# Performance work log

Hardware: AMD Instinct MI355X
Metric: run time of the kernel (lower is better)

Reference implementation:

```python
import jax, jax.numpy as jnp
import numpy as np

NUM_HEADS = 16
TOP_K = 64


def setup_inputs() -> dict:
    key = jax.random.key(0)
    ks = jax.random.split(key, 9)
    B, S, E = 2, 1024, 1024
    x = jax.random.normal(ks[0], (B, S, E), jnp.float32)
    init = lambda k: jax.random.normal(k, (E, E), jnp.float32) * 0.02
    return {
        "x": x,
        "Wq": init(ks[1]), "bq": jnp.zeros((E,), jnp.float32),
        "Wk": init(ks[2]), "bk": jnp.zeros((E,), jnp.float32),
        "Wv": init(ks[3]), "bv": jnp.zeros((E,), jnp.float32),
        "Wo": init(ks[4]), "bo": jnp.zeros((E,), jnp.float32),
    }


def reference(x, Wq, bq, Wk, bk, Wv, bv, Wo, bo):
    B, S, E = x.shape
    H = NUM_HEADS
    hd = E // H
    scale = jnp.sqrt(jnp.float32(hd))

    def proj(W, b):  # torch nn.Linear: y = x @ W^T + b -> [B,H,S,hd]
        return (x @ W.T + b).reshape(B, S, H, hd).transpose(0, 2, 1, 3)

    q = proj(Wq, bq)
    k = proj(Wk, bk)
    v = proj(Wv, bv)

    # full scores, then per-query top-k selection (same math as the torch per-i loop)
    scores = jnp.einsum('bhqd,bhkd->bhqk', q, k) / scale          # [B,H,S,S]
    top_scores, top_idx = jax.lax.top_k(scores, TOP_K)            # [B,H,S,K]

    # gather top-k values: vg[b,h,q,j,:] = v[b,h, top_idx[b,h,q,j], :]
    vg = jnp.take_along_axis(v[:, :, None, :, :], top_idx[..., None], axis=3)  # [B,H,S,K,hd]

    # torch recomputes q . gathered_k / scale, which equals top_scores exactly
    w = jax.nn.softmax(top_scores, axis=-1)                       # [B,H,S,K]
    out = jnp.einsum('bhqk,bhqkd->bhqd', w, vg)                   # [B,H,S,hd]

    out = out.transpose(0, 2, 1, 3).reshape(B, S, E)
    return out @ Wo.T + bo
```

## Files before the change

kernel.cpp:

```cpp
#include <hip/hip_runtime.h>
#include <hip/hip_bf16.h>
#include <stdint.h>


typedef __bf16 bf16_t;
typedef bf16_t bf16x8 __attribute__((ext_vector_type(8)));
typedef bf16_t bf16x4 __attribute__((ext_vector_type(4)));
typedef float  f32x4  __attribute__((ext_vector_type(4)));

#define NB 2
#define SS 1024
#define EE 1024
#define NH 16
#define HD 64
#define NBH (NB*NH)
#define NX_ ((size_t)NB*SS*EE)
#define NW_ ((size_t)EE*EE)

__device__ __forceinline__ f32x4 mfma16(bf16x8 a, bf16x8 b, f32x4 c) {
  return __builtin_amdgcn_mfma_f32_16x16x32_bf16(a, b, c, 0, 0, 0);
}

__device__ __forceinline__ void split3(float x, bf16_t& h, bf16_t& m, bf16_t& l) {
  h = (bf16_t)x;
  float r = x - (float)h;
  m = (bf16_t)r;
  float r2 = r - (float)m;
  l = (bf16_t)r2;
}

__device__ __forceinline__ void wave_fence() {
  __builtin_amdgcn_wave_barrier();
  __builtin_amdgcn_s_waitcnt(0);
  __builtin_amdgcn_wave_barrier();
}

__device__ __forceinline__ void gld16(const bf16_t* g, bf16_t* l) {
  __builtin_amdgcn_global_load_lds(
      (const __attribute__((address_space(1))) void*)g,
      (__attribute__((address_space(3))) void*)l, 16, 0, 0);
}

__global__ __launch_bounds__(256) void presplit_all(
    const float* __restrict__ x,  const float* __restrict__ wq,
    const float* __restrict__ wk, const float* __restrict__ wv,
    const float* __restrict__ wo, bf16_t* __restrict__ base)
{
  const int blk = blockIdx.x;
  const float* src; bf16_t* h; size_t n; int i;
  if (blk < 2048)      { src = x;  h = base;                   n = NX_; i = blk;        }
  else if (blk < 3072) { src = wq; h = base + 3*NX_;           n = NW_; i = blk - 2048; }
  else if (blk < 4096) { src = wk; h = base + 3*NX_ + 3*NW_;   n = NW_; i = blk - 3072; }
  else if (blk < 5120) { src = wv; h = base + 3*NX_ + 6*NW_;   n = NW_; i = blk - 4096; }
  else                 { src = wo; h = base + 3*NX_ + 9*NW_;   n = NW_; i = blk - 5120; }
  bf16_t* m = h + n;
  bf16_t* l = m + n;
  int idx = i * 256 + threadIdx.x;
  float4 v = ((const float4*)src)[idx];
  float t[4] = { v.x, v.y, v.z, v.w };
  bf16x4 hv, mv, lv;
#pragma unroll
  for (int j = 0; j < 4; j++) {
    bf16_t a, b, c;
    split3(t[j], a, b, c);
    hv[j] = a; mv[j] = b; lv[j] = c;
  }
  ((bf16x4*)h)[idx] = hv;
  ((bf16x4*)m)[idx] = mv;
  ((bf16x4*)l)[idx] = lv;
}

__global__ __launch_bounds__(256, 2) void gemm_qk(
    const bf16_t* __restrict__ Ah, const bf16_t* __restrict__ Am,
    const bf16_t* __restrict__ Al,
    const bf16_t* __restrict__ Bqh, const bf16_t* __restrict__ Bqm,
    const bf16_t* __restrict__ Bql,
    const bf16_t* __restrict__ Bkh, const bf16_t* __restrict__ Bkm,
    const bf16_t* __restrict__ Bkl,
    const float* __restrict__ biasq, const float* __restrict__ biask,
    bf16_t* __restrict__ qH, bf16_t* __restrict__ qM, bf16_t* __restrict__ qL,
    bf16_t* __restrict__ kH, bf16_t* __restrict__ kM, bf16_t* __restrict__ kL)
{
  __shared__ bf16_t As[3][128 * 32];
  __shared__ bf16_t Bs[3][64 * 32];

  const int z = blockIdx.z;
  const bf16_t* AP[3] = { Ah, Am, Al };
  const bf16_t* BP[3] = { z ? Bkh : Bqh, z ? Bkm : Bqm, z ? Bkl : Bql };
  const float* bias = z ? biask : biasq;
  bf16_t* dH = z ? kH : qH;
  bf16_t* dM = z ? kM : qM;
  bf16_t* dL = z ? kL : qL;

  const int tid  = threadIdx.x;
  const int wv   = tid >> 6, lane = tid & 63;
  const int quad = lane >> 4, l16 = lane & 15;
  const int m0 = blockIdx.y * 128, n0 = blockIdx.x * 64;
  const int wm = (wv & 1) * 64, wn = (wv >> 1) * 32;

  const int arow = wv * 32 + (lane >> 2);
  const int brow = wv * 16 + (lane >> 2);
  const int q8   = (lane & 3) * 8;
  const size_t aoff0 = (size_t)(m0 + arow) * 1024 + q8;
  const size_t boff  = (size_t)(n0 + brow) * 1024 + q8;

  f32x4 accH0[4][2] = {};
  f32x4 accH1[4][2] = {};
  f32x4 accC [4][2] = {};

  for (int k0 = 0; k0 < 1024; k0 += 32) {
    __syncthreads();
#pragma unroll
    for (int L = 0; L < 3; L++) {
      gld16(AP[L] + aoff0 + k0,              &As[L][(wv * 32) * 32]);
      gld16(AP[L] + aoff0 + 16 * 1024 + k0,  &As[L][(wv * 32 + 16) * 32]);
      gld16(BP[L] + boff + k0,               &Bs[L][(wv * 16) * 32]);
    }
    __syncthreads();

    bf16x8 bfr[2][3];
#pragma unroll
    for (int nt = 0; nt < 2; nt++)
#pragma unroll
      for (int L = 0; L < 3; L++)
        bfr[nt][L] = *(const bf16x8*)&Bs[L][(wn + nt * 16 + l16) * 32 + quad * 8];

    const bool hi = (k0 >= 512);
#pragma unroll
    for (int mt = 0; mt < 4; mt++) {
      bf16x8 af[3];
#pragma unroll
      for (int L = 0; L < 3; L++)
        af[L] = *(const bf16x8*)&As[L][(wm + mt * 16 + l16) * 32 + quad * 8];
#pragma unroll
      for (int nt = 0; nt < 2; nt++) {
        f32x4& H = hi ? accH1[mt][nt] : accH0[mt][nt];
        H = mfma16(af[0], bfr[nt][0], H);
        f32x4 c = accC[mt][nt];
        c = mfma16(af[0], bfr[nt][1], c);
        c = mfma16(af[1], bfr[nt][0], c);
        c = mfma16(af[0], bfr[nt][2], c);
        c = mfma16(af[2], bfr[nt][0], c);
        c = mfma16(af[1], bfr[nt][1], c);
        accC[mt][nt] = c;
      }
    }
  }

#pragma unroll
  for (int mt = 0; mt < 4; mt++)
#pragma unroll
  for (int nt = 0; nt < 2; nt++)
#pragma unroll
  for (int r  = 0; r  < 4;  r++) {
    int gm = m0 + wm + mt * 16 + quad * 4 + r;
    int gn = n0 + wn + nt * 16 + l16;
    float v = (accH0[mt][nt][r] + accH1[mt][nt][r]) + accC[mt][nt][r] + bias[gn];
    int b_ = gm >> 10, s_ = gm & 1023, h_ = gn >> 6, d_ = gn & 63;
    size_t di = (((size_t)b_ * NH + h_) * SS + s_) * HD + d_;
    bf16_t hh, mm, ll;
    split3(v, hh, mm, ll);
    dH[di] = hh; dM[di] = mm; dL[di] = ll;
  }
}

template<int MODE>
__global__ __launch_bounds__(256, 4) void gemm_nl2(
    const bf16_t* __restrict__ Ah, const bf16_t* __restrict__ Am,
    const bf16_t* __restrict__ Bh, const bf16_t* __restrict__ Bm,
    const float* __restrict__ bias, float* __restrict__ dF)
{
  __shared__ bf16_t As[2][64 * 32];
  __shared__ bf16_t Bs[2][64 * 32];

  const bf16_t* AP[2] = { Ah, Am };
  const bf16_t* BP[2] = { Bh, Bm };

  const int tid  = threadIdx.x;
  const int wv   = tid >> 6, lane = tid & 63;
  const int quad = lane >> 4, l16 = lane & 15;
  const int m0 = blockIdx.y * 64, n0 = blockIdx.x * 64;
  const int wm = (wv & 1) * 32, wn = (wv >> 1) * 32;

  const int srow = wv * 16 + (lane >> 2);
  const int q8   = (lane & 3) * 8;
  const size_t aoff = (size_t)(m0 + srow) * 1024 + q8;
  const size_t boff = (size_t)(n0 + srow) * 1024 + q8;

  f32x4 accH0[2][2] = {};
  f32x4 accH1[2][2] = {};
  f32x4 accC [2][2] = {};

  for (int k0 = 0; k0 < 1024; k0 += 32) {
    __syncthreads();
#pragma unroll
    for (int L = 0; L < 2; L++) {
      gld16(AP[L] + aoff + k0, &As[L][(wv * 16) * 32]);
      gld16(BP[L] + boff + k0, &Bs[L][(wv * 16) * 32]);
    }
    __syncthreads();

    bf16x8 bfr[2][2];
#pragma unroll
    for (int nt = 0; nt < 2; nt++)
#pragma unroll
      for (int L = 0; L < 2; L++)
        bfr[nt][L] = *(const bf16x8*)&Bs[L][(wn + nt * 16 + l16) * 32 + quad * 8];

    const bool hi = (k0 >= 512);
#pragma unroll
    for (int mt = 0; mt < 2; mt++) {
      bf16x8 af[2];
#pragma unroll
      for (int L = 0; L < 2; L++)
        af[L] = *(const bf16x8*)&As[L][(wm + mt * 16 + l16) * 32 + quad * 8];
#pragma unroll
      for (int nt = 0; nt < 2; nt++) {
        f32x4& H = hi ? accH1[mt][nt] : accH0[mt][nt];
        H = mfma16(af[0], bfr[nt][0], H);
        f32x4 c = accC[mt][nt];
        c = mfma16(af[0], bfr[nt][1], c);
        c = mfma16(af[1], bfr[nt][0], c);
        accC[mt][nt] = c;
      }
    }
  }

#pragma unroll
  for (int mt = 0; mt < 2; mt++)
#pragma unroll
  for (int nt = 0; nt < 2; nt++)
#pragma unroll
  for (int r  = 0; r  < 4;  r++) {
    int gm = m0 + wm + mt * 16 + quad * 4 + r;
    int gn = n0 + wn + nt * 16 + l16;
    float v = (accH0[mt][nt][r] + accH1[mt][nt][r]) + accC[mt][nt][r] + bias[gn];
    if (MODE == 2) {
      dF[(size_t)gm * 1024 + gn] = v;
    } else {
      int b_ = gm >> 10, s_ = gm & 1023, h_ = gn >> 6, d_ = gn & 63;
      dF[(((size_t)b_ * NH + h_) * SS + s_) * HD + d_] = v;
    }
  }
}

__global__ __launch_bounds__(512, 8) void attn_topk(
    const bf16_t* __restrict__ qhg, const bf16_t* __restrict__ qmg,
    const bf16_t* __restrict__ qlg,
    const bf16_t* __restrict__ khg, const bf16_t* __restrict__ kmg,
    const bf16_t* __restrict__ klg,
    const float*  __restrict__ vg,
    bf16_t* __restrict__ attnH, bf16_t* __restrict__ attnM)
{
  __shared__ float  sc[16 * 516];
  __shared__ float  selW[16 * 64];
  __shared__ ushort selI[16 * 64];

  const int tid  = threadIdx.x;
  const int wv   = tid >> 6, lane = tid & 63;
  const int quad = lane >> 4, l16 = lane & 15;
  const int xcd = blockIdx.x & 7;
  const int g   = blockIdx.x >> 3;
  const int bh  = xcd + 8 * (g >> 6);
  const int qt  = g & 63;
  const int b_ = bh >> 4, h_ = bh & 15;
  const int q0 = qt * 16;

  const size_t qbase = ((size_t)bh * SS + q0 + l16) * HD + quad * 8;
  bf16x8 aH[2], aM[2], aL[2];
#pragma unroll
  for (int ks = 0; ks < 2; ks++) {
    aH[ks] = *(const bf16x8*)(qhg + qbase + ks * 32);
    aM[ks] = *(const bf16x8*)(qmg + qbase + ks * 32);
    aL[ks] = *(const bf16x8*)(qlg + qbase + ks * 32);
  }

  float fv[2][16];
#pragma unroll
  for (int c = 0; c < 2; c++) {
    const size_t kwb = ((size_t)bh * SS + c * 512 + wv * 64 + l16) * HD + quad * 8;
#pragma unroll
    for (int t2 = 0; t2 < 4; t2++) {
      const size_t kb = kwb + (size_t)t2 * 16 * HD;
      bf16x8 bH0 = *(const bf16x8*)(khg + kb);
      bf16x8 bH1 = *(const bf16x8*)(khg + kb + 32);
      bf16x8 bM0 = *(const bf16x8*)(kmg + kb);
      bf16x8 bM1 = *(const bf16x8*)(kmg + kb + 32);
      bf16x8 bL0 = *(const bf16x8*)(klg + kb);
      bf16x8 bL1 = *(const bf16x8*)(klg + kb + 32);
      f32x4 accA = {}, accB = {}, accC = {};
      accA = mfma16(aH[0], bH0, accA);
      accB = mfma16(aH[1], bH1, accB);
      accC = mfma16(aH[0], bM0, accC);
      accC = mfma16(aH[1], bM1, accC);
      accC = mfma16(aM[0], bH0, accC);
      accC = mfma16(aM[1], bH1, accC);
      accC = mfma16(aH[0], bL0, accC);
      accC = mfma16(aH[1], bL1, accC);
      accC = mfma16(aL[0], bH0, accC);
      accC = mfma16(aL[1], bH1, accC);
      accC = mfma16(aM[0], bM0, accC);
      accC = mfma16(aM[1], bM1, accC);
      int key = wv * 64 + t2 * 16 + l16;
#pragma unroll
      for (int r = 0; r < 4; r++)
        sc[(quad * 4 + r) * 516 + key] = ((accA[r] + accB[r]) + accC[r]) * 0.125f;
    }
    __syncthreads();
#pragma unroll
    for (int i = 0; i < 8; i++) {
      fv[0][c * 8 + i] = sc[wv * 516 + i * 64 + lane];
      fv[1][c * 8 + i] = sc[(wv + 8) * 516 + i * 64 + lane];
    }
    __syncthreads();
  }

  uint32_t* bins  = (uint32_t*)sc + wv * 516;
  float*    candV = (float*)bins;
  ushort*   candI = (ushort*)(bins + 64);

  const uint64_t lt = (1ull << lane) - 1ull;
  for (int qi = 0; qi < 2; qi++) {
    int q = qi * 8 + wv;
    const float* fq = fv[qi];
    *(uint4*)(bins + lane * 8)     = uint4{0, 0, 0, 0};
    *(uint4*)(bins + lane * 8 + 4) = uint4{0, 0, 0, 0};
    wave_fence();
#pragma unroll
    for (int i = 0; i < 16; i++) {
      int b = (int)fmaxf(0.f, fminf(511.f, fmaf(fq[i], 32.f, 256.f)));
      atomicAdd(bins + b, 1u);
    }
    wave_fence();
    int base = 504 - 8 * lane;
    uint4 h0 = *(const uint4*)(bins + base);
    uint4 h1 = *(const uint4*)(bins + base + 4);
    uint32_t s_l = h0.x + h0.y + h0.z + h0.w + h1.x + h1.y + h1.z + h1.w;
    uint32_t x = s_l;
#pragma unroll
    for (int off = 1; off < 64; off <<= 1) {
      uint32_t y = __shfl_up(x, off);
      if (lane >= off) x += y;
    }
    uint32_t P = x - s_l;
    uint32_t harr[8] = { h1.w, h1.z, h1.y, h1.x, h0.w, h0.z, h0.y, h0.x };
    uint32_t cb = P, G = 0;
    int foundc = -1;
#pragma unroll
    for (int c = 0; c < 8; c++) {
      uint32_t hc = harr[c];
      if (foundc < 0 && (int)cb < 64 && (int)(cb + hc) >= 64) { foundc = c; G = cb; }
      cb += hc;
    }
    uint64_t fm = __ballot(foundc >= 0);
    int src   = __ffsll((unsigned long long)fm) - 1;
    int Bstar = __shfl((foundc >= 0) ? (511 - 8 * lane - foundc) : 0, src);
    int Gs    = __shfl((int)G, src);
    int needed = 64 - Gs;
    wave_fence();

    int pos = 0, cT = 0;
#pragma unroll
    for (int i = 0; i < 16; i++) {
      int b = (int)fmaxf(0.f, fminf(511.f, fmaf(fq[i], 32.f, 256.f)));
      bool hi = b > Bstar;
      bool cd = (b == Bstar);
      uint64_t hm = __ballot(hi);
      uint64_t em = __ballot(cd);
      int p  = pos + (int)__popcll(hm & lt);
      int cp = cT  + (int)__popcll(em & lt);
      if (hi) { selW[q * 64 + p] = fq[i]; selI[q * 64 + p] = (ushort)(i * 64 + lane); }
      if (cd && cp < 64) { candV[cp] = fq[i]; candI[cp] = (ushort)(i * 64 + lane); }
      pos += (int)__popcll(hm);
      cT  += (int)__popcll(em);
    }
    wave_fence();
    int C = cT < 64 ? cT : 64;
    float mv = candV[lane];
    int   mi = candI[lane];
    int rank = 0;
    for (int i = 0; i < C; i++) {
      float ov = candV[i]; int oi = candI[i];
      rank += (ov > mv || (ov == mv && oi < mi)) ? 1 : 0;
    }
    bool take = (lane < C) && (rank < needed);
    uint64_t tm = __ballot(take);
    int slot = Gs + (int)__popcll(tm & lt);
    if (take) { selW[q * 64 + slot] = mv; selI[q * 64 + slot] = (ushort)mi; }
    wave_fence();
    float sv = selW[q * 64 + lane];
    float mx = sv;
#pragma unroll
    for (int off = 32; off >= 1; off >>= 1) mx = fmaxf(mx, __shfl_xor(mx, off));
    float e = __expf(sv - mx);
    float sum = e;
#pragma unroll
    for (int off = 32; off >= 1; off >>= 1) sum += __shfl_xor(sum, off);
    selW[q * 64 + lane] = e / sum;
    wave_fence();
  }
  __syncthreads();

  {
    int q = tid >> 5, jh = (tid >> 4) & 1, dblk = (tid & 15) * 4;
    const float* vb = vg + (size_t)bh * SS * HD;
    f32x4 a4 = {};
#pragma unroll
    for (int bch = 0; bch < 2; bch++) {
      float wreg[16]; int ireg[16];
#pragma unroll
      for (int j = 0; j < 16; j++) {
        int jj = jh * 32 + bch * 16 + j;
        wreg[j] = selW[q * 64 + jj];
        ireg[j] = selI[q * 64 + jj];
      }
#pragma unroll
      for (int j = 0; j < 16; j++) {
        f32x4 v4 = *(const f32x4*)(vb + (size_t)ireg[j] * HD + dblk);
        a4 += wreg[j] * v4;
      }
    }
#pragma unroll
    for (int c = 0; c < 4; c++) a4[c] += __shfl_xor(a4[c], 16);
    if (jh == 0) {
      size_t dofs = ((size_t)b_ * SS + q0 + q) * EE + h_ * HD + dblk;
      bf16x4 oh, om;
#pragma unroll
      for (int j = 0; j < 4; j++) {
        bf16_t hh = (bf16_t)a4[j];
        oh[j] = hh;
        om[j] = (bf16_t)(a4[j] - (float)hh);
      }
      *(bf16x4*)(attnH + dofs) = oh;
      *(bf16x4*)(attnM + dofs) = om;
    }
  }
}

extern "C" void kernel_launch(void* const* d_in, const int* in_sizes, int n_in,
                              void* d_out, int out_size, void* d_ws, size_t ws_size,
                              hipStream_t stream)
{
  const float* x  = (const float*)d_in[0];
  const float* Wq = (const float*)d_in[1];
  const float* bq = (const float*)d_in[2];
  const float* Wk = (const float*)d_in[3];
  const float* bk = (const float*)d_in[4];
  const float* Wv = (const float*)d_in[5];
  const float* bv = (const float*)d_in[6];
  const float* Wo = (const float*)d_in[7];
  const float* bo = (const float*)d_in[8];

  bf16_t* base = (bf16_t*)d_ws;
  bf16_t *xh = base,            *xm = xh + NX_,  *xl = xm + NX_;
  bf16_t *wqh = base + 3*NX_,           *wqm = wqh + NW_, *wql = wqm + NW_;
  bf16_t *wkh = base + 3*NX_ + 3*NW_,   *wkm = wkh + NW_, *wkl = wkm + NW_;
  bf16_t *wvh = base + 3*NX_ + 6*NW_,   *wvm = wvh + NW_;
  bf16_t *woh = base + 3*NX_ + 9*NW_,   *wom = woh + NW_;
  bf16_t *p2 = base + 3*NX_ + 12*NW_;
  bf16_t *qh = p2,          *qm = qh + NX_, *ql = qm + NX_;
  bf16_t *kh = ql + NX_,    *km = kh + NX_, *kl = km + NX_;
  float  *vws = (float*)(kl + NX_);
  bf16_t *ath = (bf16_t*)(vws + NX_), *atm = ath + NX_;

  dim3 blk(256);
  presplit_all<<<dim3(6144), blk, 0, stream>>>(x, Wq, Wk, Wv, Wo, base);

  gemm_qk<<<dim3(EE / 64, (NB * SS) / 128, 2), blk, 0, stream>>>(
      xh, xm, xl, wqh, wqm, wql, wkh, wkm, wkl, bq, bk,
      qh, qm, ql, kh, km, kl);

  gemm_nl2<1><<<dim3(EE / 64, (NB * SS) / 64), blk, 0, stream>>>(
      xh, xm, wvh, wvm, bv, vws);

  attn_topk<<<dim3(NBH * (SS / 16)), dim3(512), 0, stream>>>(
      qh, qm, ql, kh, km, kl, vws, ath, atm);

  gemm_nl2<2><<<dim3(EE / 64, (NB * SS) / 64), blk, 0, stream>>>(
      ath, atm, woh, wom, bo, (float*)d_out);
}
```

Measured before the change: 381.7 us.

## Use 1024-thread blocks in attn_topk with one query per wave

The top-k attention kernel now launches 16 waves per block instead of 8. Each wave computes half as many score tiles and handles a single query in the selection phase, where before it looped over two. The value-gather phase splits the 64 selected keys four ways across lanes and reduces with two shuffles. K/Q offsets use 32-bit arithmetic. This adds intra-block parallelism and lowers per-thread register use, in exchange for larger blocks, more barrier participants and possibly lower block-level occupancy.

```diff
diff --git a/kernel.cpp b/kernel.cpp
--- a/kernel.cpp
+++ b/kernel.cpp
@@ -244,7 +244,7 @@
   }
 }
 
-__global__ __launch_bounds__(512, 8) void attn_topk(
+__global__ __launch_bounds__(1024, 4) void attn_topk(
     const bf16_t* __restrict__ qhg, const bf16_t* __restrict__ qmg,
     const bf16_t* __restrict__ qlg,
     const bf16_t* __restrict__ khg, const bf16_t* __restrict__ kmg,
@@ -266,7 +266,7 @@
   const int b_ = bh >> 4, h_ = bh & 15;
   const int q0 = qt * 16;
 
-  const size_t qbase = ((size_t)bh * SS + q0 + l16) * HD + quad * 8;
+  const uint32_t qbase = ((uint32_t)bh * SS + q0 + l16) * HD + quad * 8;
   bf16x8 aH[2], aM[2], aL[2];
 #pragma unroll
   for (int ks = 0; ks < 2; ks++) {
@@ -275,43 +275,45 @@
     aL[ks] = *(const bf16x8*)(qlg + qbase + ks * 32);
   }
 
-  float fv[2][16];
+  float fv[16];
 #pragma unroll
   for (int c = 0; c < 2; c++) {
-    const size_t kwb = ((size_t)bh * SS + c * 512 + wv * 64 + l16) * HD + quad * 8;
-#pragma unroll
-    for (int t2 = 0; t2 < 4; t2++) {
-      const size_t kb = kwb + (size_t)t2 * 16 * HD;
-      bf16x8 bH0 = *(const bf16x8*)(khg + kb);
-      bf16x8 bH1 = *(const bf16x8*)(khg + kb + 32);
-      bf16x8 bM0 = *(const bf16x8*)(kmg + kb);
-      bf16x8 bM1 = *(const bf16x8*)(kmg + kb + 32);
-      bf16x8 bL0 = *(const bf16x8*)(klg + kb);
-      bf16x8 bL1 = *(const bf16x8*)(klg + kb + 32);
-      f32x4 accA = {}, accB = {}, accC = {};
-      accA = mfma16(aH[0], bH0, accA);
-      accB = mfma16(aH[1], bH1, accB);
-      accC = mfma16(aH[0], bM0, accC);
-      accC = mfma16(aH[1], bM1, accC);
-      accC = mfma16(aM[0], bH0, accC);
-      accC = mfma16(aM[1], bH1, accC);
-      accC = mfma16(aH[0], bL0, accC);
-      accC = mfma16(aH[1], bL1, accC);
-      accC = mfma16(aL[0], bH0, accC);
-      accC = mfma16(aL[1], bH1, accC);
-      accC = mfma16(aM[0], bM0, accC);
-      accC = mfma16(aM[1], bM1, accC);
-      int key = wv * 64 + t2 * 16 + l16;
+    const uint32_t kwb = ((uint32_t)bh * SS + c * 512 + wv * 32 + l16) * HD + quad * 8;
+#pragma unroll
+    for (int t2 = 0; t2 < 2; t2++) {
+      const uint32_t kb = kwb + (uint32_t)t2 * 16 * HD;
+      f32x4 accH = {}, accC = {};
+      {
+        bf16x8 bH = *(const bf16x8*)(khg + kb);
+        bf16x8 bM = *(const bf16x8*)(kmg + kb);
+        bf16x8 bL = *(const bf16x8*)(klg + kb);
+        accH = mfma16(aH[0], bH, accH);
+        accC = mfma16(aH[0], bM, accC);
+        accC = mfma16(aM[0], bH, accC);
+        accC = mfma16(aH[0], bL, accC);
+        accC = mfma16(aL[0], bH, accC);
+        accC = mfma16(aM[0], bM, accC);
+      }
+      {
+        bf16x8 bH = *(const bf16x8*)(khg + kb + 32);
+        bf16x8 bM = *(const bf16x8*)(kmg + kb + 32);
+        bf16x8 bL = *(const bf16x8*)(klg + kb + 32);
+        accH = mfma16(aH[1], bH, accH);
+        accC = mfma16(aH[1], bM, accC);
+        accC = mfma16(aM[1], bH, accC);
+        accC = mfma16(aH[1], bL, accC);
+        accC = mfma16(aL[1], bH, accC);
+        accC = mfma16(aM[1], bM, accC);
+      }
+      int key = wv * 32 + t2 * 16 + l16;
 #pragma unroll
       for (int r = 0; r < 4; r++)
-        sc[(quad * 4 + r) * 516 + key] = ((accA[r] + accB[r]) + accC[r]) * 0.125f;
-    }
-    __syncthreads();
-#pragma unroll
-    for (int i = 0; i < 8; i++) {
-      fv[0][c * 8 + i] = sc[wv * 516 + i * 64 + lane];
-      fv[1][c * 8 + i] = sc[(wv + 8) * 516 + i * 64 + lane];
-    }
+        sc[(quad * 4 + r) * 516 + key] = (accH[r] + accC[r]) * 0.125f;
+    }
+    __syncthreads();
+#pragma unroll
+    for (int i = 0; i < 8; i++)
+      fv[c * 8 + i] = sc[wv * 516 + i * 64 + lane];
     __syncthreads();
   }
 
@@ -320,15 +322,14 @@
   ushort*   candI = (ushort*)(bins + 64);
 
   const uint64_t lt = (1ull << lane) - 1ull;
-  for (int qi = 0; qi < 2; qi++) {
-    int q = qi * 8 + wv;
-    const float* fq = fv[qi];
+  const int q = wv;
+  {
     *(uint4*)(bins + lane * 8)     = uint4{0, 0, 0, 0};
     *(uint4*)(bins + lane * 8 + 4) = uint4{0, 0, 0, 0};
     wave_fence();
 #pragma unroll
     for (int i = 0; i < 16; i++) {
-      int b = (int)fmaxf(0.f, fminf(511.f, fmaf(fq[i], 32.f, 256.f)));
+      int b = (int)fmaxf(0.f, fminf(511.f, fmaf(fv[i], 32.f, 256.f)));
       atomicAdd(bins + b, 1u);
     }
     wave_fence();
@@ -362,15 +363,15 @@
     int pos = 0, cT = 0;
 #pragma unroll
     for (int i = 0; i < 16; i++) {
-      int b = (int)fmaxf(0.f, fminf(511.f, fmaf(fq[i], 32.f, 256.f)));
+      int b = (int)fmaxf(0.f, fminf(511.f, fmaf(fv[i], 32.f, 256.f)));
       bool hi = b > Bstar;
       bool cd = (b == Bstar);
       uint64_t hm = __ballot(hi);
       uint64_t em = __ballot(cd);
       int p  = pos + (int)__popcll(hm & lt);
       int cp = cT  + (int)__popcll(em & lt);
-      if (hi) { selW[q * 64 + p] = fq[i]; selI[q * 64 + p] = (ushort)(i * 64 + lane); }
-      if (cd && cp < 64) { candV[cp] = fq[i]; candI[cp] = (ushort)(i * 64 + lane); }
+      if (hi) { selW[q * 64 + p] = fv[i]; selI[q * 64 + p] = (ushort)(i * 64 + lane); }
+      if (cd && cp < 64) { candV[cp] = fv[i]; candI[cp] = (ushort)(i * 64 + lane); }
       pos += (int)__popcll(hm);
       cT  += (int)__popcll(em);
     }
@@ -397,33 +398,32 @@
 #pragma unroll
     for (int off = 32; off >= 1; off >>= 1) sum += __shfl_xor(sum, off);
     selW[q * 64 + lane] = e / sum;
-    wave_fence();
   }
   __syncthreads();
 
   {
-    int q = tid >> 5, jh = (tid >> 4) & 1, dblk = (tid & 15) * 4;
+    int q2 = tid >> 6, jq = (tid >> 4) & 3, dblk = (tid & 15) * 4;
     const float* vb = vg + (size_t)bh * SS * HD;
     f32x4 a4 = {};
-#pragma unroll
-    for (int bch = 0; bch < 2; bch++) {
-      float wreg[16]; int ireg[16];
-#pragma unroll
-      for (int j = 0; j < 16; j++) {
-        int jj = jh * 32 + bch * 16 + j;
-        wreg[j] = selW[q * 64 + jj];
-        ireg[j] = selI[q * 64 + jj];
-      }
-#pragma unroll
-      for (int j = 0; j < 16; j++) {
-        f32x4 v4 = *(const f32x4*)(vb + (size_t)ireg[j] * HD + dblk);
-        a4 += wreg[j] * v4;
-      }
-    }
-#pragma unroll
-    for (int c = 0; c < 4; c++) a4[c] += __shfl_xor(a4[c], 16);
-    if (jh == 0) {
-      size_t dofs = ((size_t)b_ * SS + q0 + q) * EE + h_ * HD + dblk;
+    float wreg[16]; int ireg[16];
+#pragma unroll
+    for (int j = 0; j < 16; j++) {
+      int jj = jq * 16 + j;
+      wreg[j] = selW[q2 * 64 + jj];
+      ireg[j] = selI[q2 * 64 + jj];
+    }
+#pragma unroll
+    for (int j = 0; j < 16; j++) {
+      f32x4 v4 = *(const f32x4*)(vb + (size_t)ireg[j] * HD + dblk);
+      a4 += wreg[j] * v4;
+    }
+#pragma unroll
+    for (int cc = 0; cc < 4; cc++) {
+      a4[cc] += __shfl_xor(a4[cc], 16);
+      a4[cc] += __shfl_xor(a4[cc], 32);
+    }
+    if (jq == 0) {
+      size_t dofs = ((size_t)b_ * SS + q0 + q2) * EE + h_ * HD + dblk;
       bf16x4 oh, om;
 #pragma unroll
       for (int j = 0; j < 4; j++) {
@@ -473,7 +473,7 @@
   gemm_nl2<1><<<dim3(EE / 64, (NB * SS) / 64), blk, 0, stream>>>(
       xh, xm, wvh, wvm, bv, vws);
 
-  attn_topk<<<dim3(NBH * (SS / 16)), dim3(512), 0, stream>>>(
+  attn_topk<<<dim3(NBH * (SS / 16)), dim3(1024), 0, stream>>>(
       qh, qm, ql, kh, km, kl, vws, ath, atm);
 
   gemm_nl2<2><<<dim3(EE / 64, (NB * SS) / 64), blk, 0, stream>>>(
```

Measured after the change: 375.1 us. No clear change (-1.7%).
